# Kernel optimization log

Measured on AMD Instinct MI355X. Metric: run time of the kernel, lower is better.

The kernel has to match this reference:

```python
import jax, jax.numpy as jnp
import numpy as np

CONF_THRESH = 0.01
TOP_K = 200        # per-class NMS candidate cap
NMS_THRESH = 0.45
KEEP_TOP_K = 200   # global per-image cap; also output K
TEMPERATURE = 1.0
V0, V1 = 0.1, 0.2  # variances


def _nms_keep(bxs, scs):
    """Greedy NMS over candidates sorted descending by score.
    bxs: [M,4] (x1,y1,x2,y2), scs: [M] (invalid slots have score -1).
    Returns keep mask [M] (bool). Matches torch nm_suppression: a box j is
    suppressed by kept box i iff NOT (IoU(i,j) <= thresh) (NaN IoU suppresses)."""
    x1, y1, x2, y2 = bxs[:, 0], bxs[:, 1], bxs[:, 2], bxs[:, 3]
    area = (x2 - x1) * (y2 - y1)
    xx1 = jnp.maximum(x1[:, None], x1[None, :])
    yy1 = jnp.maximum(y1[:, None], y1[None, :])
    xx2 = jnp.minimum(x2[:, None], x2[None, :])
    yy2 = jnp.minimum(y2[:, None], y2[None, :])
    inter = jnp.clip(xx2 - xx1, 0.0) * jnp.clip(yy2 - yy1, 0.0)
    union = area[None, :] - inter + area[:, None]  # row i: area[i] + area[j] - inter
    iou = inter / union  # [M,M]
    M = scs.shape[0]
    valid = scs > CONF_THRESH

    def step(active, i):
        k_i = active[i]                                  # kept iff still active (sorted desc)
        sup = k_i & jnp.logical_not(iou[i] <= NMS_THRESH)
        return active & jnp.logical_not(sup), k_i

    _, keep = jax.lax.scan(step, valid, jnp.arange(M))
    return keep


def _forward(loc_data, conf_data, dbox_list):
    B, N, C = conf_data.shape
    M, K = TOP_K, KEEP_TOP_K
    # --- box decode (SSD) ---
    db = dbox_list[None]                                   # [1,N,4]
    cxcy = db[..., :2] + loc_data[..., :2] * V0 * db[..., 2:]
    wh = db[..., 2:] * jnp.exp(loc_data[..., 2:] * V1)
    mins = cxcy - wh * 0.5
    boxes = jnp.clip(jnp.concatenate([mins, mins + wh], -1), 0.0, 1.0)  # [B,N,4]
    # --- class scores ---
    probs = jax.nn.softmax(conf_data / TEMPERATURE, axis=-1)
    sc = jnp.swapaxes(probs[..., 1:], 1, 2)                # [B,C-1,N] (skip background)
    masked = jnp.where(sc > CONF_THRESH, sc, -1.0)
    top_sc, top_idx = jax.lax.top_k(masked, M)             # [B,C-1,M] desc
    cand = jnp.take_along_axis(boxes[:, None], top_idx[..., None], axis=2)  # [B,C-1,M,4]
    # --- per-class greedy NMS ---
    keep = jax.vmap(jax.vmap(_nms_keep))(cand, top_sc)     # [B,C-1,M]
    kept_sc = jnp.where(keep, top_sc, 0.0)
    # --- global keep_top_k across classes (torch topk over concatenated dets) ---
    flat = kept_sc.reshape(B, -1)
    order = jnp.argsort(-flat, axis=1)
    rank = jnp.argsort(order, axis=1)                      # inverse permutation = desc rank
    keep_g = (flat > 0.0) & (rank < K)
    fin_sc = jnp.where(keep_g, flat, 0.0).reshape(B, C - 1, M)
    fin_bx = jnp.where(keep_g.reshape(B, C - 1, M)[..., None], cand, 0.0)
    # --- per-class compaction (stable desc sort keeps NMS order among survivors) ---
    ord2 = jnp.argsort(-fin_sc, axis=2)
    sc_out = jnp.take_along_axis(fin_sc, ord2, axis=2)[..., :K]
    bx_out = jnp.take_along_axis(fin_bx, ord2[..., None], axis=2)[..., :K, :]
    body = jnp.concatenate([sc_out[..., None], bx_out], axis=-1)  # [B,C-1,K,5]
    bg = jnp.zeros((B, 1, K, 5), body.dtype)               # class 0 (background) row stays 0
    return jnp.concatenate([bg, body], axis=1)             # [B,C,K,5]


def setup_inputs() -> dict:
    key = jax.random.key(0)
    k1, k2, k3 = jax.random.split(key, 3)
    B, N, C = 8, 32768, 81
    loc_data = jax.random.normal(k1, (B, N, 4), jnp.float32)
    conf_data = jax.random.normal(k2, (B, N, C), jnp.float32)
    dbox_list = jax.random.uniform(k3, (N, 4), jnp.float32, 0.05, 0.95)  # cx,cy,w,h priors
    return {"loc_data": loc_data, "conf_data": conf_data, "dbox_list": dbox_list}


def reference(loc_data, conf_data, dbox_list):
    return _forward(loc_data, conf_data, dbox_list)
```

## Files before the change

### kernel.cpp

```cpp
#include <hip/hip_runtime.h>
#include <stdint.h>

#define CONF_T 0.01f
#define NMS_T  0.45f
#define M_TOP  200
#define TK_BS  512
#define TCAP   2048

typedef float float4u __attribute__((ext_vector_type(4), aligned(4)));

__device__ __forceinline__ uint32_t fkey(float f) {
    uint32_t u = __float_as_uint(f);
    return (u & 0x80000000u) ? ~u : (u | 0x80000000u);
}
__device__ __forceinline__ float fkey_inv(uint32_t k) {
    uint32_t u = (k & 0x80000000u) ? (k & 0x7FFFFFFFu) : ~k;
    return __uint_as_float(u);
}

__device__ __forceinline__ void suffix_select(
        uint32_t* hist, uint32_t* wsum, int nb, uint32_t pref, int shift,
        uint32_t wantv, uint32_t* s_prefix, uint32_t* s_want) {
    int tid = threadIdx.x;
    int lane = tid & 63, w = tid >> 6;
    int bpt = nb >> 8;
    int base = tid * bpt;
    uint32_t loc = 0, sfx = 0;
    if (tid < 256) {
        for (int j = 0; j < bpt; j++) loc += hist[base + j];
        sfx = loc;
        #pragma unroll
        for (int d = 1; d < 64; d <<= 1) {
            uint32_t y = __shfl_down(sfx, d);
            if (lane + d < 64) sfx += y;
        }
        if (lane == 0) wsum[w] = sfx;
    }
    __syncthreads();
    if (tid < 256) {
        uint32_t later = 0;
        for (int j = w + 1; j < 4; j++) later += wsum[j];
        uint32_t run = (sfx - loc) + later;
        for (int j = bpt - 1; j >= 0; j--) {
            uint32_t h = hist[base + j];
            uint32_t s2 = run + h;
            if (run < wantv && s2 >= wantv) {
                *s_prefix = pref | ((uint32_t)(base + j) << shift);
                *s_want   = wantv - run;
            }
            run = s2;
        }
    }
    __syncthreads();
}

__device__ __forceinline__ void suffix_select2(
        uint32_t* hist, uint32_t* wsum, int nb, uint32_t want_a, uint32_t want_b,
        uint32_t* s_bin_a, uint32_t* s_bin_b) {
    int tid = threadIdx.x;
    int lane = tid & 63, w = tid >> 6;
    int bpt = nb >> 8;
    int base = tid * bpt;
    uint32_t loc = 0, sfx = 0;
    if (tid < 256) {
        for (int j = 0; j < bpt; j++) loc += hist[base + j];
        sfx = loc;
        #pragma unroll
        for (int d = 1; d < 64; d <<= 1) {
            uint32_t y = __shfl_down(sfx, d);
            if (lane + d < 64) sfx += y;
        }
        if (lane == 0) wsum[w] = sfx;
    }
    __syncthreads();
    if (tid < 256) {
        uint32_t later = 0;
        for (int j = w + 1; j < 4; j++) later += wsum[j];
        uint32_t run = (sfx - loc) + later;
        for (int j = bpt - 1; j >= 0; j--) {
            uint32_t h = hist[base + j];
            uint32_t s2 = run + h;
            if (run < want_a && s2 >= want_a) *s_bin_a = (uint32_t)(base + j);
            if (run < want_b && s2 >= want_b) *s_bin_b = (uint32_t)(base + j);
            run = s2;
        }
    }
    __syncthreads();
}

__device__ __forceinline__ float4 decode_box(float4 l, float4 d) {
    float cx = d.x + (l.x * 0.1f) * d.z;
    float cy = d.y + (l.y * 0.1f) * d.w;
    float w  = d.z * expf(l.z * 0.2f);
    float h  = d.w * expf(l.w * 0.2f);
    float x1 = cx - w * 0.5f, y1 = cy - h * 0.5f;
    float x2 = x1 + w, y2 = y1 + h;
    float4 o;
    o.x = fminf(fmaxf(x1, 0.f), 1.f);
    o.y = fminf(fmaxf(y1, 0.f), 1.f);
    o.z = fminf(fmaxf(x2, 0.f), 1.f);
    o.w = fminf(fmaxf(y2, 0.f), 1.f);
    return o;
}

__global__ __launch_bounds__(256, 4) void softmax_kernel(
        const float* __restrict__ conf, float* __restrict__ sc,
        int* __restrict__ pcnt, int B, int N, int C) {
    int r = blockIdx.x * blockDim.x + threadIdx.x;
    if (r < B) pcnt[r] = 0;
    if (r >= B * N) return;
    const float* p = conf + (size_t)r * 81;
    float v[81];
    #pragma unroll
    for (int i = 0; i < 20; i++) {
        float4u f = *(const float4u*)(p + 4 * i);
        v[4 * i] = f.x; v[4 * i + 1] = f.y; v[4 * i + 2] = f.z; v[4 * i + 3] = f.w;
    }
    v[80] = p[80];
    float m = v[0];
    #pragma unroll
    for (int c = 1; c < 81; c++) m = fmaxf(m, v[c]);
    float s = 0.f;
    #pragma unroll
    for (int c = 0; c < 81; c++) { float e = expf(v[c] - m); v[c] = e; s += e; }
    int b = r / N, n = r % N;
    float* obase = sc + ((size_t)b * (C - 1)) * N + n;
    #pragma unroll
    for (int c = 1; c < 81; c++) obase[(size_t)(c - 1) * N] = v[c] / s;
}

__global__ __launch_bounds__(TK_BS) void topk_kernel(
        const float* __restrict__ sc, const float* __restrict__ loc,
        const float* __restrict__ dbox,
        float* __restrict__ cand,
        float* __restrict__ cmpval, int* __restrict__ cmpidx,
        int* __restrict__ pcnt,
        int B, int N, int Cm1, int M) {
    const uint32_t KEYN1 = 0x407FFFFFu;
    const uint32_t BIN_N1 = KEYN1 >> 21;
    __shared__ __align__(16) uint32_t hist[2048];
    __shared__ __align__(16) uint32_t tk[TCAP];
    __shared__ int      tix[TCAP];
    __shared__ uint32_t wsum[4];
    __shared__ uint32_t s_prefix, s_want, s_bin_a, s_bin_b;
    __shared__ uint32_t ngt, ntie, tcnt;
    __shared__ float    e_val[256];
    __shared__ int      e_idx[256];
    __shared__ int      tiebuf[256];
    __shared__ float    s_sc[M_TOP];
    __shared__ float    s_x1[M_TOP], s_y1[M_TOP], s_x2[M_TOP], s_y2[M_TOP];

    int row = blockIdx.x;
    int b = row / Cm1, c = row % Cm1;
    int tid = threadIdx.x;
    const float* v = sc + (size_t)row * N;
    const float4* v4 = (const float4*)v;
    int n4 = N >> 2;

    bool sampled = (N >= 2048) && ((N & 3) == 0);
    uint32_t lo_key = 0xFFFFFFFFu, hi_key = 0xFFFFFFFFu;
    if (sampled) {
        int stride = N >> 2;
        for (int s = 0; s < 4; s++) {
            float f = v[s * stride + tid];
            tk[s * 512 + tid] = fkey(f > CONF_T ? f : -1.0f);
        }
        for (int i = tid; i < 2048; i += TK_BS) hist[i] = 0;
        __syncthreads();
        for (int i = tid; i < 2048; i += TK_BS) atomicAdd(&hist[tk[i] >> 21], 1u);
        __syncthreads();
        suffix_select2(hist, wsum, 2048, 3u, 25u, &s_bin_a, &s_bin_b);
        uint32_t h = s_bin_a, l = s_bin_b;
        hi_key = ((h + 1) << 21) - 1u;
        lo_key = (l << 21) - 1u;
        sampled = (l > BIN_N1);
    }

    if (tid < 256) { e_val[tid] = -1.0f; e_idx[tid] = tid; }
    if (tid == 0) { ngt = 0; ntie = 0; tcnt = 0; }
    __syncthreads();

    bool ok = false;
    uint32_t G = 0, T = 0;
    if (sampled) {
        for (int i0 = tid; i0 < n4; i0 += 8 * TK_BS) {
            float4 f[8];
            #pragma unroll
            for (int u = 0; u < 8; u++) {
                int i = i0 + u * TK_BS;
                if (i < n4) f[u] = v4[i];
            }
            #pragma unroll
            for (int u = 0; u < 8; u++) {
                int i = i0 + u * TK_BS;
                if (i < n4) {
                    float mv[4] = { f[u].x > CONF_T ? f[u].x : -1.0f,
                                    f[u].y > CONF_T ? f[u].y : -1.0f,
                                    f[u].z > CONF_T ? f[u].z : -1.0f,
                                    f[u].w > CONF_T ? f[u].w : -1.0f };
                    #pragma unroll
                    for (int j = 0; j < 4; j++) {
                        uint32_t k = fkey(mv[j]);
                        if (k > lo_key) {
                            int idx = 4 * i + j;
                            if (k > hi_key) {
                                uint32_t p = atomicAdd(&ngt, 1u);
                                if (p < 256) { e_val[p] = mv[j]; e_idx[p] = idx; }
                            } else {
                                uint32_t p = atomicAdd(&tcnt, 1u);
                                if (p < TCAP) { tk[p] = k; tix[p] = idx; }
                            }
                        }
                    }
                }
            }
        }
        for (int i = (n4 << 2) + tid; i < N; i += TK_BS) {
            float f = v[i];
            float mv = f > CONF_T ? f : -1.0f;
            uint32_t k = fkey(mv);
            if (k > lo_key) {
                if (k > hi_key) {
                    uint32_t p = atomicAdd(&ngt, 1u);
                    if (p < 256) { e_val[p] = mv; e_idx[p] = i; }
                } else {
                    uint32_t p = atomicAdd(&tcnt, 1u);
                    if (p < TCAP) { tk[p] = k; tix[p] = i; }
                }
            }
        }
        __syncthreads();
        G = ngt; T = tcnt;
        ok = (G <= (uint32_t)M_TOP) && (T <= (uint32_t)TCAP) &&
             (G + T >= (uint32_t)M_TOP);
    }

    uint32_t kth = KEYN1, rfin = 0;
    if (ok) {
        uint32_t want_t = (uint32_t)M_TOP - G;
        if (want_t > 0) {
            for (int i = tid; i < 2048; i += TK_BS) hist[i] = 0;
            __syncthreads();
            for (int i = tid; i < (int)T; i += TK_BS) atomicAdd(&hist[tk[i] >> 21], 1u);
            __syncthreads();
            suffix_select(hist, wsum, 2048, 0u, 21, want_t, &s_prefix, &s_want);
            uint32_t pre0 = s_prefix, w0 = s_want;
            uint32_t bb0 = pre0 >> 21;
            for (int i = tid; i < 2048; i += TK_BS) hist[i] = 0;
            __syncthreads();
            for (int i = tid; i < (int)T; i += TK_BS)
                if ((tk[i] >> 21) == bb0) atomicAdd(&hist[(tk[i] >> 10) & 2047u], 1u);
            __syncthreads();
            suffix_select(hist, wsum, 2048, pre0, 10, w0, &s_prefix, &s_want);
            uint32_t pre1 = s_prefix, w1 = s_want;
            for (int i = tid; i < 1024; i += TK_BS) hist[i] = 0;
            __syncthreads();
            for (int i = tid; i < (int)T; i += TK_BS)
                if ((tk[i] >> 10) == (pre1 >> 10)) atomicAdd(&hist[tk[i] & 1023u], 1u);
            __syncthreads();
            suffix_select(hist, wsum, 1024, pre1, 0, w1, &s_prefix, &s_want);
            kth = s_prefix; rfin = s_want;
            for (int i = tid; i < (int)T; i += TK_BS) {
                uint32_t k = tk[i];
                if (k > kth) {
                    uint32_t p = atomicAdd(&ngt, 1u);
                    if (p < 256) { e_val[p] = fkey_inv(k); e_idx[p] = tix[i]; }
                } else if (k == kth) {
                    uint32_t p = atomicAdd(&ntie, 1u);
                    if (p < 256) tiebuf[p] = tix[i];
                }
            }
            __syncthreads();
        }
    } else {
        if (tid < 256) { e_val[tid] = -1.0f; e_idx[tid] = tid; }
        if (tid == 0) { ngt = 0; ntie = 0; tcnt = 0; }
        for (int i = tid; i < 2048; i += TK_BS) hist[i] = 0;
        __syncthreads();
        for (int i = tid; i < n4; i += TK_BS) {
            float4 f = v4[i];
            atomicAdd(&hist[fkey(f.x > CONF_T ? f.x : -1.0f) >> 21], 1u);
            atomicAdd(&hist[fkey(f.y > CONF_T ? f.y : -1.0f) >> 21], 1u);
            atomicAdd(&hist[fkey(f.z > CONF_T ? f.z : -1.0f) >> 21], 1u);
            atomicAdd(&hist[fkey(f.w > CONF_T ? f.w : -1.0f) >> 21], 1u);
        }
        for (int i = (n4 << 2) + tid; i < N; i += TK_BS)
            atomicAdd(&hist[fkey(v[i] > CONF_T ? v[i] : -1.0f) >> 21], 1u);
        __syncthreads();
        suffix_select(hist, wsum, 2048, 0u, 21, M_TOP, &s_prefix, &s_want);
        uint32_t b0 = s_prefix >> 21;
        uint32_t want1 = s_want;
        bool collect_ties = (b0 != BIN_N1);
        for (int i = tid; i < N; i += TK_BS) {
            float f = v[i];
            float mv = f > CONF_T ? f : -1.0f;
            uint32_t k = fkey(mv);
            uint32_t bin = k >> 21;
            if (bin > b0) {
                uint32_t p = atomicAdd(&ngt, 1u);
                if (p < 256) { e_val[p] = mv; e_idx[p] = i; }
            } else if (bin == b0 && collect_ties) {
                uint32_t p = atomicAdd(&tcnt, 1u);
                if (p < TCAP) { tk[p] = k; tix[p] = i; }
            }
        }
        __syncthreads();
        if (collect_ties && tcnt <= TCAP) {
            int Tl = (int)tcnt;
            for (int i = tid; i < 2048; i += TK_BS) hist[i] = 0;
            __syncthreads();
            for (int i = tid; i < Tl; i += TK_BS) atomicAdd(&hist[(tk[i] >> 10) & 2047u], 1u);
            __syncthreads();
            suffix_select(hist, wsum, 2048, b0 << 21, 10, want1, &s_prefix, &s_want);
            uint32_t pre2 = s_prefix; uint32_t want2 = s_want;
            uint32_t b1 = (pre2 >> 10) & 2047u;
            for (int i = tid; i < 1024; i += TK_BS) hist[i] = 0;
            __syncthreads();
            for (int i = tid; i < Tl; i += TK_BS)
                if (((tk[i] >> 10) & 2047u) == b1) atomicAdd(&hist[tk[i] & 1023u], 1u);
            __syncthreads();
            suffix_select(hist, wsum, 1024, pre2, 0, want2, &s_prefix, &s_want);
            kth = s_prefix; rfin = s_want;
            for (int i = tid; i < Tl; i += TK_BS) {
                uint32_t k = tk[i];
                if (k > kth) {
                    uint32_t p = atomicAdd(&ngt, 1u);
                    if (p < 256) { e_val[p] = fkey_inv(k); e_idx[p] = tix[i]; }
                } else if (k == kth) {
                    uint32_t p = atomicAdd(&ntie, 1u);
                    if (p < 256) tiebuf[p] = tix[i];
                }
            }
            __syncthreads();
        } else if (collect_ties) {
            const int shifts[2] = {10, 0};
            const int nbins_[2] = {2048, 1024};
            if (tid == 0) { s_prefix = b0 << 21; s_want = want1; }
            __syncthreads();
            for (int lev = 0; lev < 2; lev++) {
                int shift = shifts[lev];
                int nb = nbins_[lev];
                uint32_t bmask = (uint32_t)nb - 1u;
                uint32_t pref = s_prefix, wantv = s_want;
                uint32_t pmask = 0xFFFFFFFFu << (shift + ((nb == 2048) ? 11 : 10));
                for (int i = tid; i < nb; i += TK_BS) hist[i] = 0;
                __syncthreads();
                for (int i = tid; i < N; i += TK_BS) {
                    float f = v[i];
                    uint32_t k = fkey(f > CONF_T ? f : -1.0f);
                    if ((k & pmask) == (pref & pmask)) atomicAdd(&hist[(k >> shift) & bmask], 1u);
                }
                __syncthreads();
                suffix_select(hist, wsum, nb, pref, shift, wantv, &s_prefix, &s_want);
            }
            kth = s_prefix; rfin = s_want;
            for (int i = tid; i < N; i += TK_BS) {
                float f = v[i];
                float mv = f > CONF_T ? f : -1.0f;
                uint32_t k = fkey(mv);
                if ((k >> 21) == b0) {
                    if (k > kth) {
                        uint32_t p = atomicAdd(&ngt, 1u);
                        if (p < 256) { e_val[p] = mv; e_idx[p] = i; }
                    } else if (k == kth) {
                        uint32_t p = atomicAdd(&ntie, 1u);
                        if (p < 256) tiebuf[p] = i;
                    }
                }
            }
            __syncthreads();
        }
    }

    uint32_t gcount = min(ngt, (uint32_t)M_TOP);
    uint32_t nt = min(ntie, 256u);
    if (tid < (int)nt) {
        int mine = tiebuf[tid];
        uint32_t rk = 0;
        for (uint32_t j = 0; j < nt; j++) if (tiebuf[j] < mine) rk++;
        if (rk < rfin) {
            uint32_t slot = gcount + rk;
            if (slot < M_TOP) { e_val[slot] = fkey_inv(kth); e_idx[slot] = mine; }
        }
    }
    __syncthreads();
    if (tid < M_TOP) {
        float mv = e_val[tid]; int mi = e_idx[tid];
        uint32_t mk = fkey(mv);
        uint32_t rk = 0;
        for (int j = 0; j < M_TOP; j++) {
            uint32_t jk = fkey(e_val[j]); int ji = e_idx[j];
            if (jk > mk || (jk == mk && ji < mi)) rk++;
        }
        float4 l = ((const float4*)loc)[(size_t)b * N + mi];
        float4 d = ((const float4*)dbox)[mi];
        float4 bx = decode_box(l, d);
        ((float4*)cand)[(size_t)row * M_TOP + rk] = bx;
        s_sc[rk] = mv;
        s_x1[rk] = bx.x; s_y1[rk] = bx.y; s_x2[rk] = bx.z; s_y2[rk] = bx.w;
    }
    __syncthreads();

    if (tid < 64) {
        int lane = tid;
        float x1[4], y1[4], x2[4], y2[4], ar[4], sv[4];
        int act[4], kf[4];
        #pragma unroll
        for (int s = 0; s < 4; s++) {
            int j = s * 64 + lane;
            if (j < M_TOP) {
                x1[s] = s_x1[j]; y1[s] = s_y1[j]; x2[s] = s_x2[j]; y2[s] = s_y2[j];
                ar[s] = (x2[s] - x1[s]) * (y2[s] - y1[s]);
                sv[s] = s_sc[j];
            } else { x1[s]=0.f; y1[s]=0.f; x2[s]=0.f; y2[s]=0.f; ar[s]=0.f; sv[s]=-1.0f; }
            act[s] = (sv[s] > CONF_T) ? 1 : 0;
            kf[s] = 0;
        }
        #pragma unroll
        for (int si = 0; si < 4; si++) {
            int lim = M_TOP - si * 64; if (lim > 64) lim = 64;
            for (int li = 0; li < lim; li++) {
                int a = __shfl(act[si], li);
                if (a) {
                    if (lane == li) kf[si] = 1;
                    float bx1 = __shfl(x1[si], li);
                    float by1 = __shfl(y1[si], li);
                    float bx2 = __shfl(x2[si], li);
                    float by2 = __shfl(y2[si], li);
                    float bar = __shfl(ar[si], li);
                    #pragma unroll
                    for (int s = 0; s < 4; s++) {
                        float xx1 = fmaxf(bx1, x1[s]);
                        float yy1 = fmaxf(by1, y1[s]);
                        float xx2 = fminf(bx2, x2[s]);
                        float yy2 = fminf(by2, y2[s]);
                        float inter = fmaxf(xx2 - xx1, 0.f) * fmaxf(yy2 - yy1, 0.f);
                        float uni = (ar[s] - inter) + bar;
                        float iou = inter / uni;
                        if (!(iou <= NMS_T)) act[s] = 0;
                    }
                }
            }
        }
        unsigned long long ball[4];
        int total = 0;
        #pragma unroll
        for (int s = 0; s < 4; s++) { ball[s] = __ballot(kf[s] != 0); total += (int)__popcll(ball[s]); }
        int base = 0;
        if (lane == 0 && total > 0) base = atomicAdd(&pcnt[b], total);
        base = __shfl(base, 0);
        unsigned long long lower = (lane == 0) ? 0ull : (~0ull >> (64 - lane));
        int off = base;
        #pragma unroll
        for (int s = 0; s < 4; s++) {
            if (kf[s]) {
                int pos = off + (int)__popcll(ball[s] & lower);
                cmpval[(size_t)b * M + pos] = sv[s];
                cmpidx[(size_t)b * M + pos] = c * M_TOP + s * 64 + lane;
            }
            off += (int)__popcll(ball[s]);
        }
    }
}

#define GT_BS 1024
__global__ __launch_bounds__(GT_BS) void gtop_kernel(
        const float* __restrict__ cmpval, const int* __restrict__ cmpidx,
        const int* __restrict__ pcnt, float* __restrict__ gl_val,
        int* __restrict__ gl_idx, int* __restrict__ gl_cnt, int M) {
    int b = blockIdx.x;
    int tid = threadIdx.x;
    int P = pcnt[b];
    const float* cv = cmpval + (size_t)b * M;
    const int*   ci = cmpidx + (size_t)b * M;
    if (P <= M_TOP) {
        for (int i = tid; i < P; i += GT_BS) {
            gl_val[b * M_TOP + i] = cv[i];
            gl_idx[b * M_TOP + i] = ci[i];
        }
        if (tid == 0) gl_cnt[b] = P;
        return;
    }
    __shared__ uint32_t hist[256];
    __shared__ uint32_t s_prefix, s_want;
    __shared__ int tiebuf[256];
    __shared__ uint32_t ntie, wcnt;
    __shared__ int cutoff;
    if (tid == 0) { s_prefix = 0; s_want = M_TOP; }
    for (int pass = 0; pass < 4; pass++) {
        if (tid < 256) hist[tid] = 0;
        __syncthreads();
        uint32_t prefix = s_prefix;
        int shift = 24 - 8 * pass;
        for (int i = tid; i < P; i += GT_BS) {
            uint32_t k = fkey(cv[i]);
            bool ok = (pass == 0) || ((k >> (shift + 8)) == (prefix >> (shift + 8)));
            if (ok) atomicAdd(&hist[(k >> shift) & 255u], 1u);
        }
        __syncthreads();
        if (tid == 0) {
            uint32_t want = s_want, cum = 0; int bin = 0;
            for (int bb = 255; bb >= 0; bb--) {
                if (cum + hist[bb] >= want) { bin = bb; break; }
                cum += hist[bb];
            }
            s_want = want - cum;
            s_prefix = prefix | ((uint32_t)bin << shift);
        }
        __syncthreads();
    }
    uint32_t kth = s_prefix, rfin = s_want;
    if (tid == 0) { ntie = 0; cutoff = -1; wcnt = 0; }
    __syncthreads();
    for (int i = tid; i < P; i += GT_BS) {
        if (fkey(cv[i]) == kth) { uint32_t p = atomicAdd(&ntie, 1u); if (p < 256) tiebuf[p] = ci[i]; }
    }
    __syncthreads();
    uint32_t nt = min(ntie, 256u);
    if (tid < (int)nt) {
        int mine = tiebuf[tid];
        uint32_t rk = 0;
        for (uint32_t j = 0; j < nt; j++) if (tiebuf[j] < mine) rk++;
        if (rk == rfin - 1) cutoff = mine;
    }
    __syncthreads();
    int cut = cutoff;
    for (int i = tid; i < P; i += GT_BS) {
        uint32_t k = fkey(cv[i]);
        if (k > kth || (k == kth && ci[i] <= cut)) {
            uint32_t p = atomicAdd(&wcnt, 1u);
            gl_val[b * M_TOP + p] = cv[i];
            gl_idx[b * M_TOP + p] = ci[i];
        }
    }
    if (tid == 0) gl_cnt[b] = M_TOP;
}

__global__ __launch_bounds__(256) void out_kernel(
        const float* __restrict__ gl_val, const int* __restrict__ gl_idx,
        const int* __restrict__ gl_cnt, const float* __restrict__ cand,
        float* __restrict__ out, int C, int Cm1) {
    int row = blockIdx.x;
    int b = row / C, cc = row % C;
    int tid = threadIdx.x;
    size_t oslab = (size_t)row * M_TOP * 5;
    if (cc == 0) {
        float4 z; z.x = 0.f; z.y = 0.f; z.z = 0.f; z.w = 0.f;
        float4* o4 = (float4*)(out + oslab);
        for (int i = tid; i < M_TOP * 5 / 4; i += 256) o4[i] = z;
        return;
    }
    int c = cc - 1;
    __shared__ float lv[M_TOP];
    __shared__ int   lm[M_TOP];
    __shared__ uint32_t nloc;
    if (tid == 0) nloc = 0;
    __syncthreads();
    int cnt = gl_cnt[b];
    for (int i = tid; i < cnt; i += 256) {
        int idx = gl_idx[b * M_TOP + i];
        if (idx / M_TOP == c) {
            uint32_t p = atomicAdd(&nloc, 1u);
            lv[p] = gl_val[b * M_TOP + i];
            lm[p] = idx % M_TOP;
        }
    }
    __syncthreads();
    int nc = (int)nloc;
    if (tid < M_TOP) {
        if (tid < nc) {
            float v = lv[tid]; int m = lm[tid];
            int rk = 0;
            for (int j = 0; j < nc; j++)
                if (lv[j] > v || (lv[j] == v && lm[j] < m)) rk++;
            float4 bb = ((const float4*)cand)[((size_t)(b * Cm1 + c)) * M_TOP + m];
            size_t o = oslab + (size_t)rk * 5;
            out[o] = v; out[o + 1] = bb.x; out[o + 2] = bb.y;
            out[o + 3] = bb.z; out[o + 4] = bb.w;
        } else {
            size_t o = oslab + (size_t)tid * 5;
            out[o] = 0.f; out[o + 1] = 0.f; out[o + 2] = 0.f;
            out[o + 3] = 0.f; out[o + 4] = 0.f;
        }
    }
}

extern "C" void kernel_launch(void* const* d_in, const int* in_sizes, int n_in,
                              void* d_out, int out_size, void* d_ws, size_t ws_size,
                              hipStream_t stream) {
    const float* loc  = (const float*)d_in[0];
    const float* conf = (const float*)d_in[1];
    const float* dbox = (const float*)d_in[2];
    int N   = in_sizes[2] / 4;
    int B   = in_sizes[0] / (4 * N);
    int C   = in_sizes[1] / (B * N);
    int Cm1 = C - 1;
    int M   = Cm1 * M_TOP;

    char* ws = (char*)d_ws;
    size_t off = 0;
    auto alloc = [&](size_t bytes) -> char* {
        char* p = ws + off;
        off = (off + bytes + 255) & ~(size_t)255;
        return p;
    };
    float* sc     = (float*)alloc((size_t)B * Cm1 * N * sizeof(float));
    float* cand   = (float*)alloc((size_t)B * M * 4 * sizeof(float));
    int*   pcnt   = (int*)alloc((size_t)B * sizeof(int));
    float* cmpval = (float*)alloc((size_t)B * M * sizeof(float));
    int*   cmpidx = (int*)alloc((size_t)B * M * sizeof(int));
    float* gl_val = (float*)alloc((size_t)B * M_TOP * sizeof(float));
    int*   gl_idx = (int*)alloc((size_t)B * M_TOP * sizeof(int));
    int*   gl_cnt = (int*)alloc((size_t)B * sizeof(int));

    int bn = B * N;
    softmax_kernel<<<(bn + 255) / 256, 256, 0, stream>>>(conf, sc, pcnt, B, N, C);
    topk_kernel<<<B * Cm1, TK_BS, 0, stream>>>(sc, loc, dbox, cand, cmpval, cmpidx, pcnt,
                                               B, N, Cm1, M);
    gtop_kernel<<<B, GT_BS, 0, stream>>>(cmpval, cmpidx, pcnt, gl_val, gl_idx, gl_cnt, M);
    out_kernel<<<B * C, 256, 0, stream>>>(gl_val, gl_idx, gl_cnt, cand, (float*)d_out, C, Cm1);
}
```

Baseline: 270.3 us.

## Precompute NMS suppression bitmask across block and use float-compare candidate filter

Per-class NMS now starts with the whole 512-thread block computing a 200x200 IoU suppression bitmask in shared memory. A single wave then runs the greedy pass as cheap 64-bit mask ANDs instead of shuffling box coordinates and recomputing IoU serially. The candidate scan compares raw floats against precomputed float thresholds instead of building ordered keys for every element. The rank step sorts packed 64-bit key/index pairs. This trades extra parallel IoU work (computed even for suppressed boxes) for a much shorter serial dependency chain.

```diff
diff --git a/kernel.cpp b/kernel.cpp
--- a/kernel.cpp
+++ b/kernel.cpp
@@ -148,7 +148,8 @@
     __shared__ int      e_idx[256];
     __shared__ int      tiebuf[256];
     __shared__ float    s_sc[M_TOP];
-    __shared__ float    s_x1[M_TOP], s_y1[M_TOP], s_x2[M_TOP], s_y2[M_TOP];
+    __shared__ __align__(16) float4 s_bb[M_TOP];
+    __shared__ float    s_ar[M_TOP];
 
     int row = blockIdx.x;
     int b = row / Cm1, c = row % Cm1;
@@ -158,21 +159,26 @@
     int n4 = N >> 2;
 
     bool sampled = (N >= 2048) && ((N & 3) == 0);
-    uint32_t lo_key = 0xFFFFFFFFu, hi_key = 0xFFFFFFFFu;
+    float loF = 0.f, hiF = 0.f;
     if (sampled) {
         int stride = N >> 2;
+        float smp[4];
+        #pragma unroll
+        for (int s = 0; s < 4; s++) smp[s] = v[s * stride + tid];
+        for (int i = tid; i < 2048; i += TK_BS) hist[i] = 0;
+        __syncthreads();
+        #pragma unroll
         for (int s = 0; s < 4; s++) {
-            float f = v[s * stride + tid];
-            tk[s * 512 + tid] = fkey(f > CONF_T ? f : -1.0f);
-        }
-        for (int i = tid; i < 2048; i += TK_BS) hist[i] = 0;
-        __syncthreads();
-        for (int i = tid; i < 2048; i += TK_BS) atomicAdd(&hist[tk[i] >> 21], 1u);
+            float f = smp[s];
+            atomicAdd(&hist[fkey(f > CONF_T ? f : -1.0f) >> 21], 1u);
+        }
         __syncthreads();
         suffix_select2(hist, wsum, 2048, 3u, 25u, &s_bin_a, &s_bin_b);
         uint32_t h = s_bin_a, l = s_bin_b;
-        hi_key = ((h + 1) << 21) - 1u;
-        lo_key = (l << 21) - 1u;
+        uint32_t hi_key = ((h + 1) << 21) - 1u;
+        uint32_t lo_key = (l << 21) - 1u;
+        hiF = fkey_inv(hi_key);
+        loF = fmaxf(fkey_inv(lo_key), CONF_T);
         sampled = (l > BIN_N1);
     }
 
@@ -194,21 +200,18 @@
             for (int u = 0; u < 8; u++) {
                 int i = i0 + u * TK_BS;
                 if (i < n4) {
-                    float mv[4] = { f[u].x > CONF_T ? f[u].x : -1.0f,
-                                    f[u].y > CONF_T ? f[u].y : -1.0f,
-                                    f[u].z > CONF_T ? f[u].z : -1.0f,
-                                    f[u].w > CONF_T ? f[u].w : -1.0f };
+                    float e[4] = { f[u].x, f[u].y, f[u].z, f[u].w };
                     #pragma unroll
                     for (int j = 0; j < 4; j++) {
-                        uint32_t k = fkey(mv[j]);
-                        if (k > lo_key) {
+                        float fv = e[j];
+                        if (fv > loF) {
                             int idx = 4 * i + j;
-                            if (k > hi_key) {
+                            if (fv > hiF) {
                                 uint32_t p = atomicAdd(&ngt, 1u);
-                                if (p < 256) { e_val[p] = mv[j]; e_idx[p] = idx; }
+                                if (p < 256) { e_val[p] = fv; e_idx[p] = idx; }
                             } else {
                                 uint32_t p = atomicAdd(&tcnt, 1u);
-                                if (p < TCAP) { tk[p] = k; tix[p] = idx; }
+                                if (p < TCAP) { tk[p] = fkey(fv); tix[p] = idx; }
                             }
                         }
                     }
@@ -216,16 +219,14 @@
             }
         }
         for (int i = (n4 << 2) + tid; i < N; i += TK_BS) {
-            float f = v[i];
-            float mv = f > CONF_T ? f : -1.0f;
-            uint32_t k = fkey(mv);
-            if (k > lo_key) {
-                if (k > hi_key) {
+            float fv = v[i];
+            if (fv > loF) {
+                if (fv > hiF) {
                     uint32_t p = atomicAdd(&ngt, 1u);
-                    if (p < 256) { e_val[p] = mv; e_idx[p] = i; }
+                    if (p < 256) { e_val[p] = fv; e_idx[p] = i; }
                 } else {
                     uint32_t p = atomicAdd(&tcnt, 1u);
-                    if (p < TCAP) { tk[p] = k; tix[p] = i; }
+                    if (p < TCAP) { tk[p] = fkey(fv); tix[p] = i; }
                 }
             }
         }
@@ -384,68 +385,75 @@
         }
     }
     __syncthreads();
+    uint64_t* e_pack = (uint64_t*)tk;
+    if (tid < 256)
+        e_pack[tid] = ((uint64_t)fkey(e_val[tid]) << 32) | (uint32_t)~(uint32_t)e_idx[tid];
+    __syncthreads();
     if (tid < M_TOP) {
+        uint64_t mine = e_pack[tid];
+        uint32_t rk = 0;
+        for (int j = 0; j < M_TOP; j++) rk += (e_pack[j] > mine) ? 1u : 0u;
         float mv = e_val[tid]; int mi = e_idx[tid];
-        uint32_t mk = fkey(mv);
-        uint32_t rk = 0;
-        for (int j = 0; j < M_TOP; j++) {
-            uint32_t jk = fkey(e_val[j]); int ji = e_idx[j];
-            if (jk > mk || (jk == mk && ji < mi)) rk++;
-        }
         float4 l = ((const float4*)loc)[(size_t)b * N + mi];
         float4 d = ((const float4*)dbox)[mi];
         float4 bx = decode_box(l, d);
         ((float4*)cand)[(size_t)row * M_TOP + rk] = bx;
         s_sc[rk] = mv;
-        s_x1[rk] = bx.x; s_y1[rk] = bx.y; s_x2[rk] = bx.z; s_y2[rk] = bx.w;
+        s_bb[rk] = bx;
+        s_ar[rk] = (bx.z - bx.x) * (bx.w - bx.y);
+    }
+    __syncthreads();
+
+    uint64_t* sup = (uint64_t*)hist;
+    for (int task = tid; task < M_TOP * 4; task += TK_BS) {
+        int i = task >> 2, w = task & 3;
+        float4 bi = s_bb[i];
+        float ai = s_ar[i];
+        int jb = w << 6;
+        int jn = M_TOP - jb; if (jn > 64) jn = 64;
+        uint64_t m = 0;
+        for (int j = 0; j < jn; j++) {
+            float4 bj = s_bb[jb + j];
+            float xx1 = fmaxf(bi.x, bj.x);
+            float yy1 = fmaxf(bi.y, bj.y);
+            float xx2 = fminf(bi.z, bj.z);
+            float yy2 = fminf(bi.w, bj.w);
+            float inter = fmaxf(xx2 - xx1, 0.f) * fmaxf(yy2 - yy1, 0.f);
+            float uni = (s_ar[jb + j] - inter) + ai;
+            float iou = inter / uni;
+            if (!(iou <= NMS_T)) m |= (1ull << j);
+        }
+        sup[(i << 2) + w] = m;
     }
     __syncthreads();
 
     if (tid < 64) {
         int lane = tid;
-        float x1[4], y1[4], x2[4], y2[4], ar[4], sv[4];
-        int act[4], kf[4];
+        uint64_t act[4], keep[4];
         #pragma unroll
         for (int s = 0; s < 4; s++) {
-            int j = s * 64 + lane;
-            if (j < M_TOP) {
-                x1[s] = s_x1[j]; y1[s] = s_y1[j]; x2[s] = s_x2[j]; y2[s] = s_y2[j];
-                ar[s] = (x2[s] - x1[s]) * (y2[s] - y1[s]);
-                sv[s] = s_sc[j];
-            } else { x1[s]=0.f; y1[s]=0.f; x2[s]=0.f; y2[s]=0.f; ar[s]=0.f; sv[s]=-1.0f; }
-            act[s] = (sv[s] > CONF_T) ? 1 : 0;
-            kf[s] = 0;
-        }
-        #pragma unroll
-        for (int si = 0; si < 4; si++) {
-            int lim = M_TOP - si * 64; if (lim > 64) lim = 64;
-            for (int li = 0; li < lim; li++) {
-                int a = __shfl(act[si], li);
-                if (a) {
-                    if (lane == li) kf[si] = 1;
-                    float bx1 = __shfl(x1[si], li);
-                    float by1 = __shfl(y1[si], li);
-                    float bx2 = __shfl(x2[si], li);
-                    float by2 = __shfl(y2[si], li);
-                    float bar = __shfl(ar[si], li);
-                    #pragma unroll
-                    for (int s = 0; s < 4; s++) {
-                        float xx1 = fmaxf(bx1, x1[s]);
-                        float yy1 = fmaxf(by1, y1[s]);
-                        float xx2 = fminf(bx2, x2[s]);
-                        float yy2 = fminf(by2, y2[s]);
-                        float inter = fmaxf(xx2 - xx1, 0.f) * fmaxf(yy2 - yy1, 0.f);
-                        float uni = (ar[s] - inter) + bar;
-                        float iou = inter / uni;
-                        if (!(iou <= NMS_T)) act[s] = 0;
-                    }
+            int j = (s << 6) + lane;
+            float sv = (j < M_TOP) ? s_sc[j] : -1.0f;
+            act[s] = __ballot(sv > CONF_T);
+            keep[s] = 0;
+        }
+        #pragma unroll
+        for (int s = 0; s < 4; s++) {
+            int lim = M_TOP - (s << 6); if (lim > 64) lim = 64;
+            for (int bi2 = 0; bi2 < lim; bi2++) {
+                if ((act[s] >> bi2) & 1ull) {
+                    keep[s] |= (1ull << bi2);
+                    int i4 = ((s << 6) + bi2) << 2;
+                    act[0] &= ~sup[i4 + 0];
+                    act[1] &= ~sup[i4 + 1];
+                    act[2] &= ~sup[i4 + 2];
+                    act[3] &= ~sup[i4 + 3];
                 }
             }
         }
-        unsigned long long ball[4];
         int total = 0;
         #pragma unroll
-        for (int s = 0; s < 4; s++) { ball[s] = __ballot(kf[s] != 0); total += (int)__popcll(ball[s]); }
+        for (int s = 0; s < 4; s++) total += (int)__popcll(keep[s]);
         int base = 0;
         if (lane == 0 && total > 0) base = atomicAdd(&pcnt[b], total);
         base = __shfl(base, 0);
@@ -453,12 +461,12 @@
         int off = base;
         #pragma unroll
         for (int s = 0; s < 4; s++) {
-            if (kf[s]) {
-                int pos = off + (int)__popcll(ball[s] & lower);
-                cmpval[(size_t)b * M + pos] = sv[s];
-                cmpidx[(size_t)b * M + pos] = c * M_TOP + s * 64 + lane;
-            }
-            off += (int)__popcll(ball[s]);
+            if ((keep[s] >> lane) & 1ull) {
+                int pos = off + (int)__popcll(keep[s] & lower);
+                cmpval[(size_t)b * M + pos] = s_sc[(s << 6) + lane];
+                cmpidx[(size_t)b * M + pos] = c * M_TOP + (s << 6) + lane;
+            }
+            off += (int)__popcll(keep[s]);
         }
     }
 }
```

New measurement: 268.5 us, median of 2. No clear change (-0.7%).
